# Kernel tuning notes

Hardware: AMD Instinct MI355X
Metric: run time of the kernel (lower is better)

The kernel has to match this reference:

```python
import jax, jax.numpy as jnp
import numpy as np

B, S, H = 1, 4096, 2048
NH, HD = 16, 128  # num_heads, head_dim = H // NH


def setup_inputs() -> dict:
    key = jax.random.key(0)
    k1, k2, k3 = jax.random.split(key, 3)
    x = jax.random.normal(k1, (B, S, H), dtype=jnp.float32)
    w_qkv = jax.random.normal(k2, (3 * H, H), dtype=jnp.float32) * (1.0 / np.sqrt(H))
    w_out = jax.random.normal(k3, (H, H), dtype=jnp.float32) * (1.0 / np.sqrt(H))
    return {"x": x, "w_qkv": w_qkv, "w_out": w_out}


def reference(x, w_qkv, w_out):
    b, s, _ = x.shape
    # qkv projection: torch Linear computes x @ W^T
    qkv = jnp.einsum('bsh,oh->bso', x, w_qkv)
    qkv = qkv.reshape(b, s, 3, NH, HD).transpose(2, 0, 3, 1, 4)  # [3,B,NH,S,HD]
    q, k, v = qkv[0], qkv[1], qkv[2]
    # world_size == 1 -> single ring step == full attention with online softmax
    scores = jnp.einsum('bhqd,bhkd->bhqk', q, k) / np.sqrt(HD)
    m = jnp.max(scores, axis=-1, keepdims=True)          # running max (single step)
    p = jnp.exp(scores - m)                              # scores_exp
    out = jnp.einsum('bhqk,bhkd->bhqd', p, v)
    denom = jnp.sum(p, axis=-1, keepdims=True) + 1e-8    # running_sum + eps
    out = out / denom
    out = out.transpose(0, 2, 1, 3).reshape(b, s, H)     # [B,S,H]
    return jnp.einsum('bsh,oh->bso', out, w_out)
```

## Files before the change

kernel.cpp:

```cpp
#include <hip/hip_runtime.h>
#include <stdint.h>

typedef __attribute__((ext_vector_type(4))) float f32x4;
typedef __attribute__((ext_vector_type(16))) float f32x16;
typedef __attribute__((ext_vector_type(8))) short bf16x8;
typedef unsigned short u16;

#define MFMA(a, b, c) __builtin_amdgcn_mfma_f32_16x16x32_bf16(a, b, c, 0, 0, 0)
#define MFMA32(a, b, c) __builtin_amdgcn_mfma_f32_32x32x16_bf16(a, b, c, 0, 0, 0)
#define EXP2(x) __builtin_amdgcn_exp2f(x)
#define FENCE asm volatile("" ::: "memory")
#define BARRIER do { FENCE; __builtin_amdgcn_s_barrier(); FENCE; } while (0)

__device__ __forceinline__ u16 f2bf(float f) {
  union { float f; unsigned u; } x; x.f = f;
  unsigned r = x.u + 0x7fffu + ((x.u >> 16) & 1u);
  return (u16)(r >> 16);
}

__device__ __forceinline__ unsigned cvtpk(float lo, float hi) {
  unsigned r;
  asm("v_cvt_pk_bf16_f32 %0, %1, %2" : "=v"(r) : "v"(lo), "v"(hi));
  return r;
}

__device__ __forceinline__ void pl32swap(unsigned& a, unsigned& b) {
  asm volatile("v_permlane32_swap_b32 %0, %1" : "+v"(a), "+v"(b));
}

__device__ __forceinline__ void gload16(const void* g, void* l) {
  __builtin_amdgcn_global_load_lds(
      (const __attribute__((address_space(1))) unsigned int*)g,
      (__attribute__((address_space(3))) unsigned int*)l, 16, 0, 0);
}

__global__ void __launch_bounds__(256)
cast_all(const float* __restrict__ x, const float* __restrict__ wq,
         const float* __restrict__ wo, u16* __restrict__ xb,
         u16* __restrict__ wqb, u16* __restrict__ wob) {
  int idx = blockIdx.x * 256 + threadIdx.x;
  const float* in;
  u16* out;
  int j;
  if (idx < 2097152) { in = x; out = xb; j = idx; }
  else if (idx < 5242880) { in = wq; out = wqb; j = idx - 2097152; }
  else { in = wo; out = wob; j = idx - 5242880; }
  float4 v = reinterpret_cast<const float4*>(in)[j];
  ushort4 o;
  o.x = f2bf(v.x); o.y = f2bf(v.y); o.z = f2bf(v.z); o.w = f2bf(v.w);
  reinterpret_cast<ushort4*>(out)[j] = o;
}

template <int EPI>
__global__ void __launch_bounds__(512)
gemm8(const u16* __restrict__ A, const u16* __restrict__ B,
      void* __restrict__ C0, void* __restrict__ C1, void* __restrict__ C2,
      int M, int N, int K, int MBt) {
  __shared__ alignas(16) char smb[98304];
  const int tid = threadIdx.x;
  const int w = tid >> 6, lane = tid & 63;
  const int lr = lane & 15, g = lane >> 4;
  const int wm = w >> 2, wn = w & 3;
  const int gb = (blockIdx.x & 7) * ((int)gridDim.x >> 3) + (blockIdx.x >> 3);
  const int mb = gb % MBt, nb = gb / MBt;
  const int m0 = mb * 128, n0 = nb * 256;
  const int NT = K >> 6, NIT = NT >> 1;

  const int l8 = lane >> 3, l7 = lane & 7;
  const int csb = (l7 ^ l8) * 16;
  const char* asrc;
  unsigned adst;
  {
    int r = (w & 3) * 8 + ((w >> 2) << 6) + l8;
    asrc = (const char*)(A + (size_t)(m0 + r) * K) + csb;
    adst = (unsigned)(r * 128 + l7 * 16);
  }
  const char* bsrcb[2];
  unsigned bdst[2];
#pragma unroll
  for (int j = 0; j < 2; ++j) {
    int c = 2 * w + j;
    int r = (c & 3) * 8 + ((c >> 2) << 6) + l8;
    bsrcb[j] = (const char*)(B + (size_t)(n0 + r) * K) + csb;
    bdst[j] = (unsigned)(r * 128 + l7 * 16);
  }
  const size_t row32 = (size_t)32 * K * 2;

#define STG(kt, u)                                                               \
  do {                                                                           \
    if ((kt) < NT) {                                                             \
      size_t _ko = (size_t)(kt) * 128;                                           \
      int _da = ((kt) & 1) ? 16384 : 0;                                          \
      int _db = 32768 + (((kt) & 1) ? 32768 : 0);                                \
      if ((u) == 0) {                                                            \
        gload16(asrc + _ko, smb + _da + adst);                                   \
      } else if ((u) == 1) {                                                     \
        gload16(bsrcb[0] + _ko, smb + _db + bdst[0]);                            \
        gload16(bsrcb[1] + _ko, smb + _db + bdst[1]);                            \
      } else if ((u) == 2) {                                                     \
        gload16(asrc + row32 + _ko, smb + _da + 4096 + adst);                    \
      } else {                                                                   \
        gload16(bsrcb[0] + row32 + _ko, smb + _db + 4096 + bdst[0]);             \
        gload16(bsrcb[1] + row32 + _ko, smb + _db + 4096 + bdst[1]);             \
      }                                                                          \
    }                                                                            \
  } while (0)
#define VMC(n) asm volatile("s_waitcnt vmcnt(" #n ")" ::: "memory")

  f32x4 acc[4][4];
#pragma unroll
  for (int x = 0; x < 4; ++x)
#pragma unroll
    for (int y = 0; y < 4; ++y) acc[x][y] = f32x4{0.f, 0.f, 0.f, 0.f};
  bf16x8 af[2][2], bf01[2][2], bf23[2][2];
  const int aoff0 = ((g) ^ (lr & 7)) << 4;
  const int aoff1 = ((4 + g) ^ (lr & 7)) << 4;
  const int arowb = (wm * 64 + lr) * 128;
  const int browb = (wn * 64 + lr) * 128;

  auto LDA = [&](const char* base, int mih) {
#pragma unroll
    for (int mi = 0; mi < 2; ++mi) {
      const char* p = base + arowb + (mih * 32 + mi * 16) * 128;
      af[mi][0] = *(const bf16x8*)(p + aoff0);
      af[mi][1] = *(const bf16x8*)(p + aoff1);
    }
  };
  auto LDB = [&](const char* base, bf16x8 (*bfr)[2], int nih) {
#pragma unroll
    for (int ni = 0; ni < 2; ++ni) {
      const char* p = base + browb + (nih * 32 + ni * 16) * 128;
      bfr[ni][0] = *(const bf16x8*)(p + aoff0);
      bfr[ni][1] = *(const bf16x8*)(p + aoff1);
    }
  };
  auto MM = [&](int mih, int nih, bf16x8 (*bfr)[2]) {
#pragma unroll
    for (int mi = 0; mi < 2; ++mi)
#pragma unroll
      for (int ni = 0; ni < 2; ++ni) {
        acc[mih * 2 + mi][nih * 2 + ni] =
            MFMA(af[mi][0], bfr[ni][0], acc[mih * 2 + mi][nih * 2 + ni]);
        acc[mih * 2 + mi][nih * 2 + ni] =
            MFMA(af[mi][1], bfr[ni][1], acc[mih * 2 + mi][nih * 2 + ni]);
      }
  };

  STG(0, 0); STG(0, 1); STG(0, 2); STG(0, 3);
  STG(1, 0); STG(1, 1); STG(1, 3);
  VMC(5);
  BARRIER;

  const char* A0 = smb;
  const char* A1 = smb + 16384;
  const char* B0 = smb + 32768;
  const char* B1 = smb + 65536;

  for (int it = 0; it < NIT; ++it) {
    const int t0 = 2 * it;
    const bool last = (it == NIT - 1);
    LDA(A0, 0); LDB(B0, bf01, 0); LDB(B0, bf23, 1);
    STG(t0 + 1, 2);
    VMC(6);
    BARRIER;
    __builtin_amdgcn_s_setprio(1); MM(0, 0, bf01); MM(0, 1, bf23); __builtin_amdgcn_s_setprio(0);
    BARRIER;
    LDA(A0, 1);
    STG(t0 + 2, 0); STG(t0 + 2, 1); STG(t0 + 2, 3);
    if (last) VMC(1); else VMC(6);
    BARRIER;
    __builtin_amdgcn_s_setprio(1); MM(1, 1, bf23); MM(1, 0, bf01); __builtin_amdgcn_s_setprio(0);
    BARRIER;
    LDA(A1, 0); LDB(B1, bf01, 0); LDB(B1, bf23, 1);
    STG(t0 + 2, 2);
    if (last) VMC(0); else VMC(6);
    BARRIER;
    __builtin_amdgcn_s_setprio(1); MM(0, 0, bf01); MM(0, 1, bf23); __builtin_amdgcn_s_setprio(0);
    BARRIER;
    LDA(A1, 1);
    STG(t0 + 3, 0); STG(t0 + 3, 1); STG(t0 + 3, 3);
    if (last) VMC(0); else VMC(6);
    BARRIER;
    __builtin_amdgcn_s_setprio(1); MM(1, 1, bf23); MM(1, 0, bf01); __builtin_amdgcn_s_setprio(0);
    BARRIER;
  }
#undef STG
#undef VMC

  if (EPI == 0) {
    const float qs = 0.08838834764831845f * 1.4426950408889634f;
    u16* qo = (u16*)C0;
    u16* ko = (u16*)C1;
    u16* vo = (u16*)C2;
#pragma unroll
    for (int a = 0; a < 4; ++a) {
      int s0 = m0 + wm * 64 + a * 16 + g * 4;
#pragma unroll
      for (int b = 0; b < 4; ++b) {
        int n = n0 + wn * 64 + b * 16 + lr;
        int t = n >> 11, hh = (n >> 7) & 15, d = n & 127;
        if (t == 2) {
          ushort4 pk;
          pk.x = f2bf(acc[a][b][0]);
          pk.y = f2bf(acc[a][b][1]);
          pk.z = f2bf(acc[a][b][2]);
          pk.w = f2bf(acc[a][b][3]);
          *(ushort4*)(vo + (size_t)(hh * 128 + d) * 4096 + s0) = pk;
        } else {
          float sc = (t == 0) ? qs : 1.f;
          u16* dq = (t == 0 ? qo : ko) + (size_t)(hh * 4096 + s0) * 128 + d;
#pragma unroll
          for (int j = 0; j < 4; ++j) dq[(size_t)j * 128] = f2bf(acc[a][b][j] * sc);
        }
      }
    }
  } else {
    float* C = (float*)C0;
#pragma unroll
    for (int a = 0; a < 4; ++a)
#pragma unroll
      for (int b = 0; b < 4; ++b) {
        size_t r0 = (size_t)(m0 + wm * 64 + a * 16 + g * 4);
        int cn = n0 + wn * 64 + b * 16 + lr;
#pragma unroll
        for (int j = 0; j < 4; ++j) C[(r0 + j) * N + cn] = acc[a][b][j];
      }
  }
}

__global__ void __launch_bounds__(512)
attn_kernel(const u16* __restrict__ qg, const u16* __restrict__ kg,
            const u16* __restrict__ vtg, u16* __restrict__ og) {
  __shared__ alignas(64) char smb[131072];
  const int tid = threadIdx.x;
  const int w = tid >> 6, lane = tid & 63;
  const int ql = lane & 31, hl = lane >> 5;
  const int gb = (blockIdx.x & 7) * 32 + (blockIdx.x >> 3);
  const int h = gb >> 4;
  const int qb = gb & 15;

  const u16* ssrc[8];
  unsigned sdst[8];
  size_t sstep;
  if (w < 4) {
    sstep = 128 * 128;
#pragma unroll
    for (int i = 0; i < 8; ++i) {
      int c = w * 8 + i;
      int r = c * 4 + (lane >> 4);
      int sb = (lane & 15) ^ (r & 15);
      ssrc[i] = kg + (size_t)(h * 4096 + r) * 128 + sb * 8;
      sdst[i] = c * 1024;
    }
  } else {
    sstep = 128;
#pragma unroll
    for (int i = 0; i < 8; ++i) {
      int c = (w - 4) * 8 + i;
      int r = c * 4 + (lane >> 4);
      int sb = (lane & 15) ^ (r & 15);
      ssrc[i] = vtg + (size_t)(h * 128 + r) * 4096 + sb * 8;
      sdst[i] = 65536 + c * 1024;
    }
  }

  const u16* qrow = qg + (size_t)(h * 4096 + qb * 256 + w * 32 + ql) * 128 + hl * 8;
  bf16x8 qf[8];
#pragma unroll
  for (int s = 0; s < 8; ++s) qf[s] = *(const bf16x8*)(qrow + s * 16);

  f32x16 of[4];
#pragma unroll
  for (int i = 0; i < 4; ++i)
#pragma unroll
    for (int r = 0; r < 16; ++r) of[i][r] = 0.f;
  float mrun = -1e30f, lsum = 0.f;
  const float thr = 6.0f;

#pragma unroll
  for (int i = 0; i < 8; ++i) gload16(ssrc[i], smb + sdst[i]);

  const int kxor = (ql & 15) << 4;
  for (int t = 0; t < 32; ++t) {
    const int cur = t & 1;
    asm volatile("s_waitcnt vmcnt(0)" ::: "memory");
    __builtin_amdgcn_s_barrier();
    FENCE;
    if (t + 1 < 32) {
      const int nb = (t + 1) & 1;
#pragma unroll
      for (int i = 0; i < 8; ++i)
        gload16(ssrc[i] + (size_t)(t + 1) * sstep, smb + sdst[i] + nb * 32768);
    }
    const char* kbuf = smb + cur * 32768;
    const char* vbuf = smb + 65536 + cur * 32768;

    f32x16 st[4];
#pragma unroll
    for (int kb = 0; kb < 4; ++kb)
#pragma unroll
      for (int r = 0; r < 16; ++r) st[kb][r] = 0.f;
    __builtin_amdgcn_s_setprio(1);
#pragma unroll
    for (int s = 0; s < 8; ++s) {
      int off = ((s * 2 + hl) << 4) ^ kxor;
      bf16x8 k0 = *(const bf16x8*)(kbuf + (0 * 32 + ql) * 256 + off);
      bf16x8 k1 = *(const bf16x8*)(kbuf + (1 * 32 + ql) * 256 + off);
      bf16x8 k2 = *(const bf16x8*)(kbuf + (2 * 32 + ql) * 256 + off);
      bf16x8 k3 = *(const bf16x8*)(kbuf + (3 * 32 + ql) * 256 + off);
      st[0] = MFMA32(k0, qf[s], st[0]);
      st[1] = MFMA32(k1, qf[s], st[1]);
      st[2] = MFMA32(k2, qf[s], st[2]);
      st[3] = MFMA32(k3, qf[s], st[3]);
    }
    __builtin_amdgcn_s_setprio(0);

    float tmax = -1e30f;
#pragma unroll
    for (int kb = 0; kb < 4; ++kb)
#pragma unroll
      for (int r = 0; r < 16; ++r) tmax = fmaxf(tmax, st[kb][r]);
    tmax = fmaxf(tmax, __shfl_xor(tmax, 32));
    if (!__all(tmax - mrun <= thr)) {
      float mnew = fmaxf(mrun, tmax);
      float esc = EXP2(mrun - mnew);
#pragma unroll
      for (int db = 0; db < 4; ++db)
#pragma unroll
        for (int r = 0; r < 16; ++r) of[db][r] *= esc;
      lsum *= esc;
      mrun = mnew;
    }
    float psum = 0.f;
    union U { unsigned u[4]; bf16x8 v; };
    U paf[8];
#pragma unroll
    for (int gp = 0; gp < 2; ++gp) {
      unsigned pk0[8], pk1[8];
#pragma unroll
      for (int i = 0; i < 8; ++i) {
        float a0 = EXP2(st[2 * gp + 0][2 * i] - mrun);
        float b0 = EXP2(st[2 * gp + 0][2 * i + 1] - mrun);
        float a1 = EXP2(st[2 * gp + 1][2 * i] - mrun);
        float b1 = EXP2(st[2 * gp + 1][2 * i + 1] - mrun);
        psum += (a0 + b0) + (a1 + b1);
        pk0[i] = cvtpk(a0, b0);
        pk1[i] = cvtpk(a1, b1);
      }
      pl32swap(pk0[0], pk0[2]); pl32swap(pk0[1], pk0[3]);
      pl32swap(pk0[4], pk0[6]); pl32swap(pk0[5], pk0[7]);
      pl32swap(pk1[0], pk1[2]); pl32swap(pk1[1], pk1[3]);
      pl32swap(pk1[4], pk1[6]); pl32swap(pk1[5], pk1[7]);
#pragma unroll
      for (int i = 0; i < 4; ++i) {
        paf[gp * 4 + 0].u[i] = pk0[i];
        paf[gp * 4 + 1].u[i] = pk0[4 + i];
        paf[gp * 4 + 2].u[i] = pk1[i];
        paf[gp * 4 + 3].u[i] = pk1[4 + i];
      }
    }
    psum += __shfl_xor(psum, 32);
    lsum += psum;

    __builtin_amdgcn_s_setprio(1);
#pragma unroll
    for (int db = 0; db < 4; ++db) {
      const char* vrow = vbuf + (db * 32 + ql) * 256;
#pragma unroll
      for (int kp = 0; kp < 8; ++kp) {
        int m = (kp * 2 + hl) ^ (ql & 15);
        bf16x8 vf = *(const bf16x8*)(vrow + m * 16);
        of[db] = MFMA32(vf, paf[kp].v, of[db]);
      }
    }
    __builtin_amdgcn_s_setprio(0);
    FENCE;
  }

  float linv = 1.f / (lsum + 1e-8f);
  size_t qrow_o = (size_t)(qb * 256 + w * 32 + ql) * 2048 + h * 128;
#pragma unroll
  for (int db = 0; db < 4; ++db)
#pragma unroll
    for (int u = 0; u < 4; ++u) {
      ushort4 pk;
      pk.x = f2bf(of[db][4 * u + 0] * linv);
      pk.y = f2bf(of[db][4 * u + 1] * linv);
      pk.z = f2bf(of[db][4 * u + 2] * linv);
      pk.w = f2bf(of[db][4 * u + 3] * linv);
      *(ushort4*)(og + qrow_o + db * 32 + 8 * u + hl * 4) = pk;
    }
}

extern "C" void kernel_launch(void* const* d_in, const int* in_sizes, int n_in,
                              void* d_out, int out_size, void* d_ws, size_t ws_size,
                              hipStream_t stream) {
  const float* x = (const float*)d_in[0];
  const float* w_qkv = (const float*)d_in[1];
  const float* w_out = (const float*)d_in[2];

  char* ws = (char*)d_ws;
  u16* xb = (u16*)(ws + 0);
  u16* wqkvb = (u16*)(ws + 16777216);
  u16* woutb = (u16*)(ws + 41943040);
  u16* qb = (u16*)(ws + 50331648);
  u16* kb = (u16*)(ws + 67108864);
  u16* vtb = (u16*)(ws + 83886080);
  u16* aob = (u16*)(ws + 100663296);

  cast_all<<<24576, 256, 0, stream>>>(x, w_qkv, w_out, xb, wqkvb, woutb);
  gemm8<0><<<768, 512, 0, stream>>>(xb, wqkvb, qb, kb, vtb, 4096, 6144, 2048, 32);
  attn_kernel<<<256, 512, 0, stream>>>(qb, kb, vtb, aob);
  gemm8<1><<<256, 512, 0, stream>>>(aob, woutb, d_out, nullptr, nullptr, 4096, 2048, 2048, 32);
}
```

Measured before the change: 312.9 us.

## Add dedicated 128x384-tile QKV GEMM kernel replacing 128x256 gemm8 path

Introduces a new gemm384 kernel for the QKV projection that uses 128x384 output tiles (512 blocks instead of 768), with its own double-buffered LDS staging where the B tile is loaded in two halves interleaved with MFMA compute. The aim is more reuse of each A tile per block, and a grid of 512 blocks that maps onto the 256 CUs as exactly two waves. It uses 128KB of LDS and 96 accumulator registers per thread, which raises register pressure and could lower occupancy. The output epilogue is moved out of gemm8, which now only handles the fp32 output projection.

```diff
diff --git a/kernel.cpp b/kernel.cpp
--- a/kernel.cpp
+++ b/kernel.cpp
@@ -49,6 +49,174 @@
   ushort4 o;
   o.x = f2bf(v.x); o.y = f2bf(v.y); o.z = f2bf(v.z); o.w = f2bf(v.w);
   reinterpret_cast<ushort4*>(out)[j] = o;
+}
+
+__global__ void __launch_bounds__(512)
+gemm384(const u16* __restrict__ A, const u16* __restrict__ B,
+        u16* __restrict__ qo, u16* __restrict__ ko, u16* __restrict__ vo, int K) {
+  __shared__ alignas(16) char smb[131072];
+  const int tid = threadIdx.x;
+  const int w = tid >> 6, lane = tid & 63;
+  const int lr = lane & 15, g = lane >> 4;
+  const int wm = w >> 2, wn = w & 3;
+  const int gb = (blockIdx.x & 7) * 64 + (blockIdx.x >> 3);
+  const int mb = gb & 31, nb = gb >> 5;
+  const int m0 = mb * 128, n0 = nb * 384;
+  const int NT = K >> 6;
+
+  const int l8 = lane >> 3, l7 = lane & 7;
+  const int csb = (l7 ^ l8) * 16;
+  const char* asrc[2];
+  unsigned adst[2];
+#pragma unroll
+  for (int j = 0; j < 2; ++j) {
+    int c = 2 * w + j;
+    int r = c * 8 + l8;
+    asrc[j] = (const char*)(A + (size_t)(m0 + r) * K) + csb;
+    adst[j] = (unsigned)(r * 128 + l7 * 16);
+  }
+  const char* b1src[3];
+  const char* b2src[3];
+  unsigned b1dst[3], b2dst[3];
+#pragma unroll
+  for (int j = 0; j < 3; ++j) {
+    int c = 3 * w + j;
+    int blk = c / 6, sub = c % 6;
+    int r1 = blk * 96 + sub * 8 + l8;
+    int r2 = r1 + 48;
+    b1src[j] = (const char*)(B + (size_t)(n0 + r1) * K) + csb;
+    b1dst[j] = (unsigned)(r1 * 128 + l7 * 16);
+    b2src[j] = (const char*)(B + (size_t)(n0 + r2) * K) + csb;
+    b2dst[j] = (unsigned)(r2 * 128 + l7 * 16);
+  }
+
+#define STGA(kt)                                                        \
+  do {                                                                  \
+    if ((kt) < NT) {                                                    \
+      size_t _ko = (size_t)(kt) * 128;                                  \
+      int _da = ((kt) & 1) ? 16384 : 0;                                 \
+      gload16(asrc[0] + _ko, smb + _da + adst[0]);                      \
+      gload16(asrc[1] + _ko, smb + _da + adst[1]);                      \
+    }                                                                   \
+  } while (0)
+#define STGB1(kt)                                                       \
+  do {                                                                  \
+    if ((kt) < NT) {                                                    \
+      size_t _ko = (size_t)(kt) * 128;                                  \
+      int _db = 32768 + (((kt) & 1) ? 49152 : 0);                       \
+      gload16(b1src[0] + _ko, smb + _db + b1dst[0]);                    \
+      gload16(b1src[1] + _ko, smb + _db + b1dst[1]);                    \
+      gload16(b1src[2] + _ko, smb + _db + b1dst[2]);                    \
+    }                                                                   \
+  } while (0)
+#define STGB2(kt)                                                       \
+  do {                                                                  \
+    if ((kt) < NT) {                                                    \
+      size_t _ko = (size_t)(kt) * 128;                                  \
+      int _db = 32768 + (((kt) & 1) ? 49152 : 0);                       \
+      gload16(b2src[0] + _ko, smb + _db + b2dst[0]);                    \
+      gload16(b2src[1] + _ko, smb + _db + b2dst[1]);                    \
+      gload16(b2src[2] + _ko, smb + _db + b2dst[2]);                    \
+    }                                                                   \
+  } while (0)
+#define VMC(n) asm volatile("s_waitcnt vmcnt(" #n ")" ::: "memory")
+
+  f32x4 acc[4][6];
+#pragma unroll
+  for (int a = 0; a < 4; ++a)
+#pragma unroll
+    for (int b = 0; b < 6; ++b) acc[a][b] = f32x4{0.f, 0.f, 0.f, 0.f};
+  bf16x8 af[4][2], bf[3][2];
+  const int aoff0 = ((g) ^ (lr & 7)) << 4;
+  const int aoff1 = ((4 + g) ^ (lr & 7)) << 4;
+  const int arow = (wm * 64 + lr) * 128;
+  const int brow = (wn * 96 + lr) * 128;
+
+  STGA(0); STGB1(0); STGB2(0);
+  STGA(1); STGB1(1);
+  VMC(8);
+  BARRIER;
+
+  for (int t = 0; t < 32; ++t) {
+    const char* Ab = smb + ((t & 1) ? 16384 : 0);
+    const char* Bb = smb + 32768 + ((t & 1) ? 49152 : 0);
+
+#pragma unroll
+    for (int a = 0; a < 4; ++a) {
+      const char* p = Ab + arow + a * 2048;
+      af[a][0] = *(const bf16x8*)(p + aoff0);
+      af[a][1] = *(const bf16x8*)(p + aoff1);
+    }
+#pragma unroll
+    for (int nk = 0; nk < 3; ++nk) {
+      const char* p = Bb + brow + nk * 2048;
+      bf[nk][0] = *(const bf16x8*)(p + aoff0);
+      bf[nk][1] = *(const bf16x8*)(p + aoff1);
+    }
+    STGB2(t + 1);
+    if (t == 31) VMC(0); else VMC(8);
+    BARRIER;
+    __builtin_amdgcn_s_setprio(1);
+#pragma unroll
+    for (int a = 0; a < 4; ++a)
+#pragma unroll
+      for (int nk = 0; nk < 3; ++nk) {
+        acc[a][nk] = MFMA(af[a][0], bf[nk][0], acc[a][nk]);
+        acc[a][nk] = MFMA(af[a][1], bf[nk][1], acc[a][nk]);
+      }
+    __builtin_amdgcn_s_setprio(0);
+    BARRIER;
+
+#pragma unroll
+    for (int nk = 0; nk < 3; ++nk) {
+      const char* p = Bb + brow + (48 * 128) + nk * 2048;
+      bf[nk][0] = *(const bf16x8*)(p + aoff0);
+      bf[nk][1] = *(const bf16x8*)(p + aoff1);
+    }
+    STGA(t + 2); STGB1(t + 2);
+    if (t == 30) VMC(3);
+    else if (t == 31) VMC(0);
+    else VMC(8);
+    BARRIER;
+    __builtin_amdgcn_s_setprio(1);
+#pragma unroll
+    for (int a = 0; a < 4; ++a)
+#pragma unroll
+      for (int nk = 0; nk < 3; ++nk) {
+        acc[a][3 + nk] = MFMA(af[a][0], bf[nk][0], acc[a][3 + nk]);
+        acc[a][3 + nk] = MFMA(af[a][1], bf[nk][1], acc[a][3 + nk]);
+      }
+    __builtin_amdgcn_s_setprio(0);
+    BARRIER;
+  }
+#undef STGA
+#undef STGB1
+#undef STGB2
+#undef VMC
+
+  const float qs = 0.08838834764831845f * 1.4426950408889634f;
+#pragma unroll
+  for (int a = 0; a < 4; ++a) {
+    int s0 = m0 + wm * 64 + a * 16 + g * 4;
+#pragma unroll
+    for (int b = 0; b < 6; ++b) {
+      int n = n0 + wn * 96 + b * 16 + lr;
+      int t = n >> 11, hh = (n >> 7) & 15, d = n & 127;
+      if (t == 2) {
+        ushort4 pk;
+        pk.x = f2bf(acc[a][b][0]);
+        pk.y = f2bf(acc[a][b][1]);
+        pk.z = f2bf(acc[a][b][2]);
+        pk.w = f2bf(acc[a][b][3]);
+        *(ushort4*)(vo + (size_t)(hh * 128 + d) * 4096 + s0) = pk;
+      } else {
+        float sc = (t == 0) ? qs : 1.f;
+        u16* dq = (t == 0 ? qo : ko) + (size_t)(hh * 4096 + s0) * 128 + d;
+#pragma unroll
+        for (int j = 0; j < 4; ++j) dq[(size_t)j * 128] = f2bf(acc[a][b][j] * sc);
+      }
+    }
+  }
 }
 
 template <int EPI>
@@ -187,45 +355,16 @@
 #undef STG
 #undef VMC
 
-  if (EPI == 0) {
-    const float qs = 0.08838834764831845f * 1.4426950408889634f;
-    u16* qo = (u16*)C0;
-    u16* ko = (u16*)C1;
-    u16* vo = (u16*)C2;
-#pragma unroll
-    for (int a = 0; a < 4; ++a) {
-      int s0 = m0 + wm * 64 + a * 16 + g * 4;
-#pragma unroll
-      for (int b = 0; b < 4; ++b) {
-        int n = n0 + wn * 64 + b * 16 + lr;
-        int t = n >> 11, hh = (n >> 7) & 15, d = n & 127;
-        if (t == 2) {
-          ushort4 pk;
-          pk.x = f2bf(acc[a][b][0]);
-          pk.y = f2bf(acc[a][b][1]);
-          pk.z = f2bf(acc[a][b][2]);
-          pk.w = f2bf(acc[a][b][3]);
-          *(ushort4*)(vo + (size_t)(hh * 128 + d) * 4096 + s0) = pk;
-        } else {
-          float sc = (t == 0) ? qs : 1.f;
-          u16* dq = (t == 0 ? qo : ko) + (size_t)(hh * 4096 + s0) * 128 + d;
-#pragma unroll
-          for (int j = 0; j < 4; ++j) dq[(size_t)j * 128] = f2bf(acc[a][b][j] * sc);
-        }
-      }
-    }
-  } else {
-    float* C = (float*)C0;
-#pragma unroll
-    for (int a = 0; a < 4; ++a)
-#pragma unroll
-      for (int b = 0; b < 4; ++b) {
-        size_t r0 = (size_t)(m0 + wm * 64 + a * 16 + g * 4);
-        int cn = n0 + wn * 64 + b * 16 + lr;
-#pragma unroll
-        for (int j = 0; j < 4; ++j) C[(r0 + j) * N + cn] = acc[a][b][j];
-      }
-  }
+  float* C = (float*)C0;
+#pragma unroll
+  for (int a = 0; a < 4; ++a)
+#pragma unroll
+    for (int b = 0; b < 4; ++b) {
+      size_t r0 = (size_t)(m0 + wm * 64 + a * 16 + g * 4);
+      int cn = n0 + wn * 64 + b * 16 + lr;
+#pragma unroll
+      for (int j = 0; j < 4; ++j) C[(r0 + j) * N + cn] = acc[a][b][j];
+    }
 }
 
 __global__ void __launch_bounds__(512)
@@ -409,7 +548,7 @@
   u16* aob = (u16*)(ws + 100663296);
 
   cast_all<<<24576, 256, 0, stream>>>(x, w_qkv, w_out, xb, wqkvb, woutb);
-  gemm8<0><<<768, 512, 0, stream>>>(xb, wqkvb, qb, kb, vtb, 4096, 6144, 2048, 32);
+  gemm384<<<512, 512, 0, stream>>>(xb, wqkvb, qb, kb, vtb, 2048);
   attn_kernel<<<256, 512, 0, stream>>>(qb, kb, vtb, aob);
   gemm8<1><<<256, 512, 0, stream>>>(aob, woutb, d_out, nullptr, nullptr, 4096, 2048, 2048, 32);
 }
```

After: 304.5 us, median of 2. 2.7% less time.
